# Optimization experiments

Measured on AMD Instinct MI355X. Metric: run time of the kernel, lower is better.

## Reference

```python
import jax, jax.numpy as jnp
import numpy as np

N = 100000
DIN = 896        # 128 * 7, hard-coded as input_dim1 in hccexplorer_graph
HID = 256        # hidden_channels
HEADS = 1        # num_heads
L = 2            # num_layers
ALPHA = 0.5
EPS = 1e-5


def layernorm(x, g, b):
    m = jnp.mean(x, axis=-1, keepdims=True)
    v = jnp.mean((x - m) ** 2, axis=-1, keepdims=True)
    return (x - m) / jnp.sqrt(v + EPS) * g + b


def full_attention_conv(qs, ks, vs):
    # qs, ks, vs: [N, H, D]. NOTE: global Frobenius-norm normalization (no dim arg in torch.norm).
    n = qs.shape[0]
    qs = qs / jnp.linalg.norm(qs)
    ks = ks / jnp.linalg.norm(ks)
    kvs = jnp.einsum('lhm,lhd->hmd', ks, vs)                 # [H, D, D]
    attn_num = jnp.einsum('nhm,hmd->nhd', qs, kvs) + n * vs  # [N, H, D]
    ks_sum = jnp.sum(ks, axis=0)                             # [H, D]
    denom = jnp.einsum('nhm,hm->nh', qs, ks_sum)[..., None] + n
    return attn_num / denom                                  # [N, H, D]


def setup_inputs() -> dict:
    key = jax.random.key(0)
    ks = jax.random.split(key, 12)
    s_in = 1.0 / np.sqrt(DIN)
    s_h = 1.0 / np.sqrt(HID)
    inp = {
        'x': jax.random.normal(ks[0], (N, DIN), jnp.float32),
        'edge_index': jax.random.randint(ks[1], (2, 1600000), 0, N, jnp.int64),
        'fc_w': jax.random.uniform(ks[2], (DIN, HID), jnp.float32, -s_in, s_in),
        'fc_b': jax.random.uniform(ks[3], (HID,), jnp.float32, -s_in, s_in),
        'Wq': jax.random.uniform(ks[4], (L, HID, HEADS * HID), jnp.float32, -s_h, s_h),
        'Wk': jax.random.uniform(ks[5], (L, HID, HEADS * HID), jnp.float32, -s_h, s_h),
        'Wv': jax.random.uniform(ks[6], (L, HID, HEADS * HID), jnp.float32, -s_h, s_h),
        'bq': jax.random.uniform(ks[7], (L, HEADS * HID), jnp.float32, -s_h, s_h),
        'bk': jax.random.uniform(ks[8], (L, HEADS * HID), jnp.float32, -s_h, s_h),
        'bv': jax.random.uniform(ks[9], (L, HEADS * HID), jnp.float32, -s_h, s_h),
        'ln_g': 1.0 + 0.01 * jax.random.normal(ks[10], (L + 1, HID), jnp.float32),
        'ln_b': 0.01 * jax.random.normal(ks[11], (L + 1, HID), jnp.float32),
    }
    return inp


def reference(x, edge_index, fc_w, fc_b, Wq, Wk, Wv, bq, bk, bv, ln_g, ln_b):
    # TransConv.forward in eval mode (dropout disabled); edge_index unused by linear attention.
    h = x @ fc_w + fc_b
    h = layernorm(h, ln_g[0], ln_b[0])
    h = jax.nn.relu(h)
    prev = h
    for i in range(L):
        q = (h @ Wq[i] + bq[i]).reshape(-1, HEADS, HID)
        k = (h @ Wk[i] + bk[i]).reshape(-1, HEADS, HID)
        v = (h @ Wv[i] + bv[i]).reshape(-1, HEADS, HID)
        a = full_attention_conv(q, k, v).mean(axis=1)        # [N, HID]
        h = ALPHA * a + (1.0 - ALPHA) * prev                  # residual
        h = layernorm(h, ln_g[i + 1], ln_b[i + 1])
        prev = h
    return h
```

## Files before the change

kernel.cpp:

```cpp
#include <hip/hip_runtime.h>
#include <hip/hip_bf16.h>

typedef __attribute__((ext_vector_type(8))) __bf16 bf16x8;
typedef __attribute__((ext_vector_type(4))) float floatx4;

__device__ __forceinline__ bf16x8 cvt8(float4 a, float4 b) {
    bf16x8 w;
    w[0] = (__bf16)a.x; w[1] = (__bf16)a.y; w[2] = (__bf16)a.z; w[3] = (__bf16)a.w;
    w[4] = (__bf16)b.x; w[5] = (__bf16)b.y; w[6] = (__bf16)b.z; w[7] = (__bf16)b.w;
    return w;
}

__global__ void __launch_bounds__(256) prep_kernel(
    const float* __restrict__ fc_w, const float* __restrict__ Wv,
    __bf16* __restrict__ fcwT, __bf16* __restrict__ WvT)
{
    int idx = blockIdx.x * 256 + threadIdx.x;
    if (idx < 229376) {
        int k32 = idx >> 13, rem = idx & 8191;
        int t = rem >> 9, q = (rem >> 7) & 3, c = (rem >> 3) & 15, e = rem & 7;
        int n = t * 16 + c, k = k32 * 32 + q * 8 + e;
        fcwT[idx] = (__bf16)fc_w[k * 256 + n];
    } else {
        int j = idx - 229376;
        int l = j >> 16, r = j & 65535;
        int k32 = r >> 13, rem = r & 8191;
        int t = rem >> 9, q = (rem >> 7) & 3, c = (rem >> 3) & 15, e = rem & 7;
        int n = t * 16 + c, k = k32 * 32 + q * 8 + e;
        WvT[j] = (__bf16)Wv[l * 65536 + k * 256 + n];
    }
}

template<int MODE>
__device__ __forceinline__ void ln_epilogue(
    floatx4 (&acc)[4][4],
    const float* __restrict__ bias, const float* __restrict__ g,
    const float* __restrict__ bb, __bf16* sH, float2* sScr,
    float* __restrict__ Out, int m0, int M, int tid)
{
    const int wave = tid >> 6, lane = tid & 63;
    const int q = lane >> 4, c15 = lane & 15;

    float bj[4];
#pragma unroll
    for (int j = 0; j < 4; ++j) bj[j] = bias[wave * 64 + j * 16 + c15];
#pragma unroll
    for (int i = 0; i < 4; ++i)
#pragma unroll
        for (int r = 0; r < 4; ++r) {
            int rl = i * 16 + q * 4 + r;
#pragma unroll
            for (int j = 0; j < 4; ++j) {
                float v = acc[i][j][r] + bj[j];
                if (MODE != 0) {
                    int col = wave * 64 + j * 16 + c15;
                    int byte = rl * 512 + (((col >> 3) ^ (rl & 7)) << 4) + ((col & 7) << 1);
                    float pv = (float)*(const __bf16*)((const char*)sH + byte);
                    v = 0.5f * v + 0.5f * pv;
                }
                acc[i][j][r] = v;
            }
        }

    float s[4][4], s2[4][4];
#pragma unroll
    for (int i = 0; i < 4; ++i)
#pragma unroll
        for (int r = 0; r < 4; ++r) {
            float t = 0.f, t2 = 0.f;
#pragma unroll
            for (int j = 0; j < 4; ++j) { float v = acc[i][j][r]; t += v; t2 += v * v; }
            s[i][r] = t; s2[i][r] = t2;
        }
#pragma unroll
    for (int m = 1; m < 16; m <<= 1)
#pragma unroll
        for (int i = 0; i < 4; ++i)
#pragma unroll
            for (int r = 0; r < 4; ++r) {
                s[i][r]  += __shfl_xor(s[i][r],  m);
                s2[i][r] += __shfl_xor(s2[i][r], m);
            }

    float2* part  = sScr;
    float2* muinv = sScr + 256;
    if (c15 == 0) {
#pragma unroll
        for (int i = 0; i < 4; ++i)
#pragma unroll
            for (int r = 0; r < 4; ++r) {
                int rl = i * 16 + q * 4 + r;
                part[rl * 4 + wave] = make_float2(s[i][r], s2[i][r]);
            }
    }
    __syncthreads();
    if (tid < 64) {
        float S = 0.f, SS = 0.f;
#pragma unroll
        for (int w = 0; w < 4; ++w) { float2 p = part[tid * 4 + w]; S += p.x; SS += p.y; }
        float mu  = S * (1.f / 256.f);
        float var = SS * (1.f / 256.f) - mu * mu;
        muinv[tid] = make_float2(mu, rsqrtf(var + 1e-5f));
    }
    __syncthreads();

    float gj[4], bj2[4];
#pragma unroll
    for (int j = 0; j < 4; ++j) {
        int col = wave * 64 + j * 16 + c15;
        gj[j] = g[col]; bj2[j] = bb[col];
    }
#pragma unroll
    for (int i = 0; i < 4; ++i)
#pragma unroll
        for (int r = 0; r < 4; ++r) {
            int rl = i * 16 + q * 4 + r;
            float2 mi = muinv[rl];
#pragma unroll
            for (int j = 0; j < 4; ++j) {
                float y = (acc[i][j][r] - mi.x) * mi.y * gj[j] + bj2[j];
                if (MODE == 0) y = fmaxf(y, 0.f);
                int col = wave * 64 + j * 16 + c15;
                if (MODE < 2) {
                    int byte = rl * 512 + (((col >> 3) ^ (rl & 7)) << 4) + ((col & 7) << 1);
                    *(__bf16*)((char*)sH + byte) = (__bf16)y;
                } else {
                    int row = m0 + rl;
                    if (row < M) Out[(size_t)row * 256 + col] = y;
                }
            }
        }
}

__global__ void __launch_bounds__(256, 3) fused_net(
    const float* __restrict__ x, const __bf16* __restrict__ fcwT,
    const __bf16* __restrict__ WvT, const float* __restrict__ fc_b,
    const float* __restrict__ bv, const float* __restrict__ ln_g,
    const float* __restrict__ ln_b, float* __restrict__ Out, int M)
{
    __shared__ __align__(16) __bf16 sA[2][64 * 32];
    __shared__ __align__(16) __bf16 sH[64 * 256];
    __shared__ __align__(16) float2 sScr[320];

    const int tid  = threadIdx.x;
    const int wave = tid >> 6, lane = tid & 63;
    const int m0   = blockIdx.x * 64;
    const int lrow = lane & 15;
    const int q4   = lane >> 4;
    const int srow = tid >> 2;
    const int scol = (tid & 3) * 8;
    int aRow = m0 + srow; if (aRow > M - 1) aRow = M - 1;

    const int sw    = (tid & 3) ^ ((srow >> 1) & 3);
    const int aWoff = srow * 64 + (sw << 4);
    const int fslot = (q4 ^ ((lrow >> 1) & 3)) << 4;
    const int hx    = lrow & 7;

    floatx4 acc[4][4];
#pragma unroll
    for (int i = 0; i < 4; ++i)
#pragma unroll
        for (int j = 0; j < 4; ++j) acc[i][j] = {0.f, 0.f, 0.f, 0.f};

    bf16x8 bF[4], bFn[4];

    {
        const int K = 896;
        const __bf16* bPtr = fcwT + wave * 2048 + lane * 8;
#pragma unroll
        for (int j = 0; j < 4; ++j) bF[j] = *(const bf16x8*)(bPtr + j * 512);
        {
            const float* src = x + (size_t)aRow * K + scol;
            float4 p0 = *(const float4*)src, p1 = *(const float4*)(src + 4);
            *(bf16x8*)((char*)sA[0] + aWoff) = cvt8(p0, p1);
        }

        for (int it = 0; it < 28; ++it) {
            const int cur = it & 1, nxt = cur ^ 1;
            __syncthreads();
            const bool more = (it + 1 < 28);
            float4 p0, p1;
            if (more) {
                const float* src = x + (size_t)aRow * K + ((it + 1) << 5) + scol;
                p0 = *(const float4*)src; p1 = *(const float4*)(src + 4);
#pragma unroll
                for (int j = 0; j < 4; ++j)
                    bFn[j] = *(const bf16x8*)(bPtr + (it + 1) * 8192 + j * 512);
            }
            bf16x8 aF[4];
#pragma unroll
            for (int i = 0; i < 4; ++i)
                aF[i] = *(const bf16x8*)((char*)sA[cur] + (i * 16 + lrow) * 64 + fslot);
#pragma unroll
            for (int i = 0; i < 4; ++i)
#pragma unroll
                for (int j = 0; j < 4; ++j)
                    acc[i][j] = __builtin_amdgcn_mfma_f32_16x16x32_bf16(aF[i], bF[j], acc[i][j], 0, 0, 0);
            if (more) {
                *(bf16x8*)((char*)sA[nxt] + aWoff) = cvt8(p0, p1);
#pragma unroll
                for (int j = 0; j < 4; ++j) bF[j] = bFn[j];
            }
        }
        ln_epilogue<0>(acc, fc_b, ln_g, ln_b, sH, sScr, nullptr, m0, M, tid);
    }

#pragma unroll
    for (int l = 0; l < 2; ++l) {
        const __bf16* bPtr = WvT + l * 65536 + wave * 2048 + lane * 8;
#pragma unroll
        for (int i = 0; i < 4; ++i)
#pragma unroll
            for (int j = 0; j < 4; ++j) acc[i][j] = {0.f, 0.f, 0.f, 0.f};
#pragma unroll
        for (int j = 0; j < 4; ++j) bF[j] = *(const bf16x8*)(bPtr + j * 512);

        __syncthreads();

        for (int it = 0; it < 8; ++it) {
            if (it < 7) {
#pragma unroll
                for (int j = 0; j < 4; ++j)
                    bFn[j] = *(const bf16x8*)(bPtr + (it + 1) * 8192 + j * 512);
            }
            bf16x8 aF[4];
            const int ks = (it << 2) + q4;
#pragma unroll
            for (int i = 0; i < 4; ++i)
                aF[i] = *(const bf16x8*)((char*)sH + (i * 16 + lrow) * 512 + ((ks ^ hx) << 4));
#pragma unroll
            for (int i = 0; i < 4; ++i)
#pragma unroll
                for (int j = 0; j < 4; ++j)
                    acc[i][j] = __builtin_amdgcn_mfma_f32_16x16x32_bf16(aF[i], bF[j], acc[i][j], 0, 0, 0);
            if (it < 7) {
#pragma unroll
                for (int j = 0; j < 4; ++j) bF[j] = bFn[j];
            }
        }

        if (l == 0)
            ln_epilogue<1>(acc, bv, ln_g + 256, ln_b + 256, sH, sScr, nullptr, m0, M, tid);
        else
            ln_epilogue<2>(acc, bv + 256, ln_g + 512, ln_b + 512, sH, sScr, Out, m0, M, tid);
    }
}

extern "C" void kernel_launch(void* const* d_in, const int* in_sizes, int n_in,
                              void* d_out, int out_size, void* d_ws, size_t ws_size,
                              hipStream_t stream)
{
    const float* x    = (const float*)d_in[0];
    const float* fc_w = (const float*)d_in[2];
    const float* fc_b = (const float*)d_in[3];
    const float* Wv   = (const float*)d_in[6];
    const float* bv   = (const float*)d_in[9];
    const float* ln_g = (const float*)d_in[10];
    const float* ln_b = (const float*)d_in[11];

    const int M = in_sizes[0] / 896;

    char* ws = (char*)d_ws;
    __bf16* fcwT = (__bf16*)ws;
    __bf16* WvT  = (__bf16*)(ws + 458752);

    prep_kernel<<<1408, 256, 0, stream>>>(fc_w, Wv, fcwT, WvT);

    const int nblk = (M + 63) / 64;
    fused_net<<<nblk, 256, 0, stream>>>(x, fcwT, WvT, fc_b, bv, ln_g, ln_b,
                                        (float*)d_out, M);
}
```

Measured before the change: 717.5 us.

## Raise occupancy via LDS aliasing, deepen x prefetch, nontemporal output stores

The LayerNorm scratch buffer now aliases the A staging buffer instead of taking its own shared memory. Together with raising the launch-bounds minimum from 3 to 4 blocks, this is meant to let four blocks share a CU. The first GEMM loop is unrolled by two with explicit ping-pong buffers, and x is prefetched into registers two K-steps ahead to hide global-load latency better. Final outputs are written with nontemporal stores to avoid polluting the cache. The risk is that the tighter register budget at higher occupancy, plus the extra prefetch registers, causes spills.

```diff
diff --git a/kernel.cpp b/kernel.cpp
--- a/kernel.cpp
+++ b/kernel.cpp
@@ -126,13 +126,14 @@
                     *(__bf16*)((char*)sH + byte) = (__bf16)y;
                 } else {
                     int row = m0 + rl;
-                    if (row < M) Out[(size_t)row * 256 + col] = y;
+                    if (row < M)
+                        __builtin_nontemporal_store(y, &Out[(size_t)row * 256 + col]);
                 }
             }
         }
 }
 
-__global__ void __launch_bounds__(256, 3) fused_net(
+__global__ void __launch_bounds__(256, 4) fused_net(
     const float* __restrict__ x, const __bf16* __restrict__ fcwT,
     const __bf16* __restrict__ WvT, const float* __restrict__ fc_b,
     const float* __restrict__ bv, const float* __restrict__ ln_g,
@@ -140,7 +141,7 @@
 {
     __shared__ __align__(16) __bf16 sA[2][64 * 32];
     __shared__ __align__(16) __bf16 sH[64 * 256];
-    __shared__ __align__(16) float2 sScr[320];
+    float2* sScr = (float2*)sA;
 
     const int tid  = threadIdx.x;
     const int wave = tid >> 6, lane = tid & 63;
@@ -165,39 +166,67 @@
     bf16x8 bF[4], bFn[4];
 
     {
-        const int K = 896;
+        const float* xp = x + (size_t)aRow * 896 + scol;
         const __bf16* bPtr = fcwT + wave * 2048 + lane * 8;
 #pragma unroll
         for (int j = 0; j < 4; ++j) bF[j] = *(const bf16x8*)(bPtr + j * 512);
         {
-            const float* src = x + (size_t)aRow * K + scol;
-            float4 p0 = *(const float4*)src, p1 = *(const float4*)(src + 4);
+            float4 p0 = *(const float4*)xp, p1 = *(const float4*)(xp + 4);
             *(bf16x8*)((char*)sA[0] + aWoff) = cvt8(p0, p1);
         }
-
-        for (int it = 0; it < 28; ++it) {
-            const int cur = it & 1, nxt = cur ^ 1;
+        float4 Xa0 = *(const float4*)(xp + 32), Xa1 = *(const float4*)(xp + 36);
+        float4 Xb0, Xb1;
+
+        for (int t = 0; t < 14; ++t) {
+            const int it = 2 * t;
             __syncthreads();
-            const bool more = (it + 1 < 28);
-            float4 p0, p1;
-            if (more) {
-                const float* src = x + (size_t)aRow * K + ((it + 1) << 5) + scol;
-                p0 = *(const float4*)src; p1 = *(const float4*)(src + 4);
+            const bool m2 = (it + 2 < 28);
+            if (m2) {
+                const float* s2p = xp + (it + 2) * 32;
+                Xb0 = *(const float4*)s2p; Xb1 = *(const float4*)(s2p + 4);
+            }
+#pragma unroll
+            for (int j = 0; j < 4; ++j)
+                bFn[j] = *(const bf16x8*)(bPtr + (it + 1) * 8192 + j * 512);
+            {
+                bf16x8 aF[4];
+#pragma unroll
+                for (int i = 0; i < 4; ++i)
+                    aF[i] = *(const bf16x8*)((char*)sA[0] + (i * 16 + lrow) * 64 + fslot);
+                *(bf16x8*)((char*)sA[1] + aWoff) = cvt8(Xa0, Xa1);
+#pragma unroll
+                for (int i = 0; i < 4; ++i)
+#pragma unroll
+                    for (int j = 0; j < 4; ++j)
+                        acc[i][j] = __builtin_amdgcn_mfma_f32_16x16x32_bf16(aF[i], bF[j], acc[i][j], 0, 0, 0);
+            }
+#pragma unroll
+            for (int j = 0; j < 4; ++j) bF[j] = bFn[j];
+
+            __syncthreads();
+            if (it + 3 < 28) {
+                const float* s3p = xp + (it + 3) * 32;
+                Xa0 = *(const float4*)s3p; Xa1 = *(const float4*)(s3p + 4);
+            }
+            if (m2) {
 #pragma unroll
                 for (int j = 0; j < 4; ++j)
-                    bFn[j] = *(const bf16x8*)(bPtr + (it + 1) * 8192 + j * 512);
-            }
-            bf16x8 aF[4];
-#pragma unroll
-            for (int i = 0; i < 4; ++i)
-                aF[i] = *(const bf16x8*)((char*)sA[cur] + (i * 16 + lrow) * 64 + fslot);
-#pragma unroll
-            for (int i = 0; i < 4; ++i)
-#pragma unroll
-                for (int j = 0; j < 4; ++j)
-                    acc[i][j] = __builtin_amdgcn_mfma_f32_16x16x32_bf16(aF[i], bF[j], acc[i][j], 0, 0, 0);
-            if (more) {
-                *(bf16x8*)((char*)sA[nxt] + aWoff) = cvt8(p0, p1);
+                    bFn[j] = *(const bf16x8*)(bPtr + (it + 2) * 8192 + j * 512);
+            }
+            {
+                bf16x8 aF[4];
+#pragma unroll
+                for (int i = 0; i < 4; ++i)
+                    aF[i] = *(const bf16x8*)((char*)sA[1] + (i * 16 + lrow) * 64 + fslot);
+                if (m2)
+                    *(bf16x8*)((char*)sA[0] + aWoff) = cvt8(Xb0, Xb1);
+#pragma unroll
+                for (int i = 0; i < 4; ++i)
+#pragma unroll
+                    for (int j = 0; j < 4; ++j)
+                        acc[i][j] = __builtin_amdgcn_mfma_f32_16x16x32_bf16(aF[i], bF[j], acc[i][j], 0, 0, 0);
+            }
+            if (m2) {
 #pragma unroll
                 for (int j = 0; j < 4; ++j) bF[j] = bFn[j];
             }
```

New measurement: 792.6 us. 10.5% more time.
